# Optimization experiments

Measured on AMD Instinct MI355X. Metric: run time of the kernel, lower is better.

## Reference

```python
import jax, jax.numpy as jnp
import numpy as np


def _knn_graph(x, k):
    """Faithful port of DynamicLstmGnn.knn_to_graph + get_u_v, returning the
    dense symmetrized edge-weight matrix [N, N] (the original re-sparsifies
    this same matrix via coalesce; nonzero extraction is data-dependent and
    not jit-able, so the dense matrix is the canonical output)."""
    N = x.shape[0]
    # negative squared euclidean distance: -||xi||^2 + 2 xi.xj - ||xj||^2
    xx = jnp.sum(x * x, axis=1, keepdims=True)          # [N, 1]
    inner = -2.0 * (x @ x.T)                              # [N, N]
    pairwise_distance = -xx - inner - xx.T                # [N, N], <= 0
    vals, idx = jax.lax.top_k(pairwise_distance, k)       # [N, k] largest (= closest)
    rows = jnp.repeat(jnp.arange(N), k)                   # idx_prime.flatten()
    # sparse COO -> to_dense (duplicate indices sum, matching torch.sparse)
    edges = jnp.zeros((N, N), dtype=x.dtype).at[rows, idx.ravel()].add(vals.ravel())
    edges_int = (edges > 0).astype(x.dtype)
    reflected_int = edges_int + edges_int.T
    reflected_edges = edges + edges.T
    denom = jnp.where(reflected_int == 0, jnp.ones((), x.dtype), reflected_int)
    edges = reflected_edges / denom
    diag = jnp.arange(N)
    edges = edges.at[diag, diag].set(0.0)                 # fill_diagonal_(0)
    return edges


def setup_inputs() -> dict:
    key = jax.random.key(0)
    x = jax.random.normal(key, (10000, 64), dtype=jnp.float32)
    return {"x": x, "k": 5}


def reference(x, k):
    return _knn_graph(x, k)
```

## Files before the change

kernel.cpp:

```cpp
#include <hip/hip_runtime.h>

#define D 64
#define K 5
#define LK 8
#define GK 12
#define NSPLIT 16
#define NTILES 625
#define ROWBLK 157
#define NCOMP (ROWBLK * NSPLIT)
typedef unsigned int u32;
typedef unsigned long long u64;
typedef __bf16 bf16x8 __attribute__((ext_vector_type(8)));
typedef float  f32x4v __attribute__((ext_vector_type(4)));

__device__ __forceinline__ u32 med3u(u32 a, u32 b, u32 c) {
    u32 r;
    asm("v_med3_u32 %0, %1, %2, %3" : "=v"(r) : "v"(a), "v"(b), "v"(c));
    return r;
}

__device__ __forceinline__ u32 pack32(float v, int idx) {
    u32 u = __float_as_uint(v);
    u ^= ((u32)((int)u >> 31)) | 0x80000000u;
    return (u & 0xFFFFC000u) | ((~(u32)idx) & 0x3FFFu);
}
__device__ __forceinline__ int idx32(u32 key) { return (int)((~key) & 0x3FFFu); }

__device__ __forceinline__ u64 packKV(float v, int idx) {
    u32 u = __float_as_uint(v);
    u ^= ((u32)((int)u >> 31)) | 0x80000000u;
    return ((u64)u << 32) | (u32)(~idx);
}
__device__ __forceinline__ float unpackV(u64 key) {
    u32 hu = (u32)(key >> 32);
    return (hu & 0x80000000u) ? __uint_as_float(hu & 0x7fffffffu)
                              : __uint_as_float(~hu);
}

template<int LO, int LA, int LB, typename T>
__device__ __forceinline__ void mergeKeep(T a[LA], const T b[LB]) {
    T A[LA], B[LB], out[LO];
#pragma unroll
    for (int i = 0; i < LA; ++i) A[i] = a[i];
#pragma unroll
    for (int i = 0; i < LB; ++i) B[i] = b[i];
#pragma unroll
    for (int m = 0; m < LO; ++m) {
        bool ta = A[0] >= B[0];
        out[m] = ta ? A[0] : B[0];
#pragma unroll
        for (int i = 0; i < LA - 1; ++i) A[i] = ta ? A[i + 1] : A[i];
        A[LA - 1] = ta ? (T)0 : A[LA - 1];
#pragma unroll
        for (int i = 0; i < LB - 1; ++i) B[i] = ta ? B[i] : B[i + 1];
        B[LB - 1] = ta ? B[LB - 1] : (T)0;
    }
#pragma unroll
    for (int m = 0; m < LO; ++m) a[m] = out[m];
}

__global__ __launch_bounds__(256) void prep(
    const float* __restrict__ x, __bf16* __restrict__ xbA, float* __restrict__ xxf, int N)
{
    int g = blockIdx.x * 256 + threadIdx.x;
    const int REPACK = NTILES * 2 * 64;
    if (g < REPACK) {
        int tile = g >> 7;
        int rem  = g & 127;
        int kh   = rem >> 6;
        int lane = rem & 63;
        int q = lane >> 4, r = lane & 15;
        int row = tile * 16 + r;
        int k0  = kh * 32 + q * 8;
        const float4* p = (const float4*)(x + (size_t)row * D + k0);
        float4 v0 = p[0], v1 = p[1];
        bf16x8 o;
        o[0] = (__bf16)v0.x; o[1] = (__bf16)v0.y; o[2] = (__bf16)v0.z; o[3] = (__bf16)v0.w;
        o[4] = (__bf16)v1.x; o[5] = (__bf16)v1.y; o[6] = (__bf16)v1.z; o[7] = (__bf16)v1.w;
        ((bf16x8*)xbA)[g] = o;
        return;
    }
    int i = g - REPACK;
    if (i >= N) return;
    const float4* p = (const float4*)(x + (size_t)i * D);
    float s = 0.f;
#pragma unroll
    for (int t = 0; t < 16; ++t) {
        float4 v = p[t];
        s += v.x * v.x + v.y * v.y + v.z * v.z + v.w * v.w;
    }
    xxf[i] = s;
}

__global__ __launch_bounds__(256, 6) void topk_zero_mfma(
    const __bf16* __restrict__ xbA, const float* __restrict__ xxf, int N,
    u32* __restrict__ wsK, float* __restrict__ outZ, long long totalF4,
    int nZero, int f4PerZ)
{
    const int bx  = blockIdx.x;
    const int tid = threadIdx.x;
    const int g8  = bx >> 3;
    const int r8  = bx & 7;

    if (g8 % 6 == 0) {
        int zid = (g8 / 6) * 8 + r8;
        if (zid >= nZero) return;
        long long s = (long long)zid * f4PerZ;
        long long e = s + f4PerZ; if (e > totalF4) e = totalF4;
        const f32x4v z = {0.f, 0.f, 0.f, 0.f};
        for (long long i = s + tid; i < e; i += 256)
            __builtin_nontemporal_store(z, (f32x4v*)(outZ + 4 * i));
        return;
    }

    const int cid = bx - (g8 / 6 + 1) * 8;
    if (cid >= NCOMP) return;
    const int split = cid / ROWBLK;
    const int rb    = cid - split * ROWBLK;

    const int lane = tid & 63;
    const int wave = tid >> 6;
    const int l15  = lane & 15;
    const int q    = lane >> 4;
    const int r0 = rb * 64 + wave * 16;

    const bf16x8* fb = (const bf16x8*)xbA;

    int bt = r0 >> 4; if (bt > NTILES - 1) bt = NTILES - 1;
    const bf16x8 B0 = fb[bt * 128 + lane];
    const bf16x8 B1 = fb[bt * 128 + 64 + lane];

    const bf16x8* ap = fb + (size_t)split * 128 + lane;
    const float* xcp = xxf + split * 16 + q * 4;
    int cbase = split * 16 + q * 4;
    const int apBump = NSPLIT * 128;
    const int xcBump = NSPLIT * 16;

    u32 L[LK];
#pragma unroll
    for (int m = 0; m < LK; ++m) L[m] = 0u;

    bf16x8 A0a = ap[0];
    bf16x8 A1a = ap[64];
    f32x4v xca = *(const f32x4v*)xcp;
    ap += apBump; xcp += xcBump;
    bf16x8 A0b = ap[0];
    bf16x8 A1b = ap[64];
    f32x4v xcb = *(const f32x4v*)xcp;

    for (int t = split; t < NTILES; t += NSPLIT) {
        ap += apBump; xcp += xcBump;
        const bf16x8 nA0 = ap[0];
        const bf16x8 nA1 = ap[64];
        const f32x4v nxc = *(const f32x4v*)xcp;

        f32x4v acc0 = {0.f, 0.f, 0.f, 0.f};
        f32x4v acc1 = {0.f, 0.f, 0.f, 0.f};
        acc0 = __builtin_amdgcn_mfma_f32_16x16x32_bf16(A0a, B0, acc0, 0, 0, 0);
        acc1 = __builtin_amdgcn_mfma_f32_16x16x32_bf16(A1a, B1, acc1, 0, 0, 0);

#pragma unroll
        for (int v = 0; v < 4; ++v) {
            float dk = fmaf(-0.5f, xca[v], acc0[v] + acc1[v]);
            u32 key = pack32(dk, cbase + v);
            u32 n0 = max(L[0], key);
            u32 n1 = med3u(L[0], L[1], key);
            u32 n2 = med3u(L[1], L[2], key);
            u32 n3 = med3u(L[2], L[3], key);
            u32 n4 = med3u(L[3], L[4], key);
            u32 n5 = med3u(L[4], L[5], key);
            u32 n6 = med3u(L[5], L[6], key);
            u32 n7 = med3u(L[6], L[7], key);
            L[0]=n0; L[1]=n1; L[2]=n2; L[3]=n3; L[4]=n4; L[5]=n5; L[6]=n6; L[7]=n7;
        }
        cbase += xcBump;
        A0a = A0b; A1a = A1b; xca = xcb;
        A0b = nA0; A1b = nA1; xcb = nxc;
    }

#pragma unroll
    for (int mask = 16; mask <= 32; mask <<= 1) {
        u32 P[LK];
#pragma unroll
        for (int m = 0; m < LK; ++m) P[m] = (u32)__shfl_xor((int)L[m], mask);
        mergeKeep<LK, LK, LK, u32>(L, P);
    }

    if (lane < 16) {
        int row = r0 + l15;
        if (row < N) {
            u32* dst = wsK + ((size_t)row * NSPLIT + split) * LK;
#pragma unroll
            for (int m = 0; m < LK; ++m) dst[m] = L[m];
        }
    }
}

__global__ __launch_bounds__(256) void rescore_scatter(
    const u32* __restrict__ wsK, const float* __restrict__ x, const float* __restrict__ xxf,
    float* __restrict__ out, int N)
{
    const int lane = threadIdx.x & 63;
    const int wave = threadIdx.x >> 6;
    const int sub  = lane & 3;
    const int row  = blockIdx.x * 64 + wave * 16 + (lane >> 2);
    const bool vrow = (row < N);
    const int rr = vrow ? row : 0;

    u32 cur[GK];
    {
        const u32* Lp = wsK + ((size_t)rr * NSPLIT + 4 * sub) * LK;
#pragma unroll
        for (int m = 0; m < LK; ++m) cur[m] = Lp[m];
#pragma unroll
        for (int m = LK; m < GK; ++m) cur[m] = 0u;
#pragma unroll
        for (int l = 1; l < 4; ++l) {
            u32 b[LK];
#pragma unroll
            for (int m = 0; m < LK; ++m) b[m] = Lp[l * LK + m];
            mergeKeep<GK, GK, LK, u32>(cur, b);
        }
    }
#pragma unroll
    for (int mask = 1; mask <= 2; mask <<= 1) {
        u32 P[GK];
#pragma unroll
        for (int m = 0; m < GK; ++m) P[m] = (u32)__shfl_xor((int)cur[m], mask);
        mergeKeep<GK, GK, GK, u32>(cur, P);
    }

    const float nxi = xxf[rr];
    int   cj[3]; bool cval[3];
    float d[3] = {0.f, 0.f, 0.f};
    const f32x4v* pj[3];
#pragma unroll
    for (int c = 0; c < 3; ++c) {
        int j = idx32(cur[sub * 3 + c]);
        cval[c] = (j < N) && (cur[sub * 3 + c] != 0u);
        cj[c] = cval[c] ? j : 0;
        pj[c] = (const f32x4v*)(x + (size_t)cj[c] * D);
    }
    const f32x4v* xip = (const f32x4v*)(x + (size_t)rr * D);
#pragma unroll
    for (int t = 0; t < 16; ++t) {
        const f32x4v xv = xip[t];
#pragma unroll
        for (int c = 0; c < 3; ++c) {
            const f32x4v pv = pj[c][t];
            d[c] = fmaf(xv[0], pv[0], d[c]);
            d[c] = fmaf(xv[1], pv[1], d[c]);
            d[c] = fmaf(xv[2], pv[2], d[c]);
            d[c] = fmaf(xv[3], pv[3], d[c]);
        }
    }
    u64 F[K];
#pragma unroll
    for (int c = 0; c < 3; ++c) {
        float val = 2.f * d[c] - nxi - xxf[cj[c]];
        F[c] = cval[c] ? packKV(val, cj[c]) : 0ull;
    }
    F[3] = 0ull; F[4] = 0ull;
    { u64 a0=F[0],a1=F[1],a2=F[2];
      if (a0 < a1) { u64 t0=a0; a0=a1; a1=t0; }
      if (a1 < a2) { u64 t0=a1; a1=a2; a2=t0; }
      if (a0 < a1) { u64 t0=a0; a0=a1; a1=t0; }
      F[0]=a0; F[1]=a1; F[2]=a2; }
#pragma unroll
    for (int mask = 1; mask <= 2; mask <<= 1) {
        u64 P[K];
#pragma unroll
        for (int m = 0; m < K; ++m) P[m] = __shfl_xor(F[m], mask);
        mergeKeep<K, K, K, u64>(F, P);
    }

    if (sub == 0 && vrow) {
#pragma unroll
        for (int m = 0; m < K; ++m) {
            int j = (int)(~(u32)F[m]);
            if ((unsigned)j < (unsigned)N && j != row) {
                float v = unpackV(F[m]);
                atomicAdd(out + (size_t)row * N + j, v);
                atomicAdd(out + (size_t)j * N + row, v);
            }
        }
    }
}

extern "C" void kernel_launch(void* const* d_in, const int* in_sizes, int n_in,
                              void* d_out, int out_size, void* d_ws, size_t ws_size,
                              hipStream_t stream) {
    const float* x = (const float*)d_in[0];
    const int N = in_sizes[0] / D;
    float* out = (float*)d_out;

    const size_t oXB = 0;
    const size_t oXX = 0x150000;
    const size_t oWK = 0x160000;
    __bf16* xbA = (__bf16*)((char*)d_ws + oXB);
    float*  xxf = (float*)((char*)d_ws + oXX);
    u32*    wsK = (u32*)((char*)d_ws + oWK);

    const int prepThreads = NTILES * 2 * 64 + N;
    prep<<<(prepThreads + 255) / 256, 256, 0, stream>>>(x, xbA, xxf, N);

    long long totalF4 = (long long)out_size / 4;
    const int nBlocksTotal = 3024;
    const int nZero = 504;
    int f4PerZ = (int)((totalF4 + nZero - 1) / nZero);
    topk_zero_mfma<<<nBlocksTotal, 256, 0, stream>>>(
        xbA, xxf, N, wsK, out, totalF4, nZero, f4PerZ);

    rescore_scatter<<<ROWBLK, 256, 0, stream>>>(wsK, x, xxf, out, N);
}
```

Measured before the change: 451.2 us.

## Seed MFMA accumulator with -0.5*norm and chain both MFMAs into one accumulator

Prep now also writes a precomputed -0.5*||x||^2 array, which the top-k kernel uses as the initial MFMA accumulator. The two MFMAs chain into that single accumulator, which removes the separate add and fma per element. The packed key index is built incrementally from a decreasing base instead of through pack32. The double-buffered prefetch is cut to a single stage. The launch-bounds occupancy hint of 6 is dropped, and the zero-fill uses plain stores instead of nontemporal ones. The chained MFMAs add a dependency, which may expose MFMA latency now that the prefetch is shallower.

```diff
diff --git a/kernel.cpp b/kernel.cpp
--- a/kernel.cpp
+++ b/kernel.cpp
@@ -60,7 +60,8 @@
 }
 
 __global__ __launch_bounds__(256) void prep(
-    const float* __restrict__ x, __bf16* __restrict__ xbA, float* __restrict__ xxf, int N)
+    const float* __restrict__ x, __bf16* __restrict__ xbA,
+    float* __restrict__ xxf, float* __restrict__ xxh, int N)
 {
     int g = blockIdx.x * 256 + threadIdx.x;
     const int REPACK = NTILES * 2 * 64;
@@ -90,10 +91,11 @@
         s += v.x * v.x + v.y * v.y + v.z * v.z + v.w * v.w;
     }
     xxf[i] = s;
-}
-
-__global__ __launch_bounds__(256, 6) void topk_zero_mfma(
-    const __bf16* __restrict__ xbA, const float* __restrict__ xxf, int N,
+    xxh[i] = -0.5f * s;
+}
+
+__global__ __launch_bounds__(256) void topk_zero_mfma(
+    const __bf16* __restrict__ xbA, const float* __restrict__ xxh, int N,
     u32* __restrict__ wsK, float* __restrict__ outZ, long long totalF4,
     int nZero, int f4PerZ)
 {
@@ -109,7 +111,7 @@
         long long e = s + f4PerZ; if (e > totalF4) e = totalF4;
         const f32x4v z = {0.f, 0.f, 0.f, 0.f};
         for (long long i = s + tid; i < e; i += 256)
-            __builtin_nontemporal_store(z, (f32x4v*)(outZ + 4 * i));
+            *(f32x4v*)(outZ + 4 * i) = z;
         return;
     }
 
@@ -131,8 +133,8 @@
     const bf16x8 B1 = fb[bt * 128 + 64 + lane];
 
     const bf16x8* ap = fb + (size_t)split * 128 + lane;
-    const float* xcp = xxf + split * 16 + q * 4;
-    int cbase = split * 16 + q * 4;
+    const float* xhp = xxh + split * 16 + q * 4;
+    u32 base16k = 0x3FFFu - (u32)(split * 16 + q * 4);
     const int apBump = NSPLIT * 128;
     const int xcBump = NSPLIT * 16;
 
@@ -140,29 +142,25 @@
 #pragma unroll
     for (int m = 0; m < LK; ++m) L[m] = 0u;
 
-    bf16x8 A0a = ap[0];
-    bf16x8 A1a = ap[64];
-    f32x4v xca = *(const f32x4v*)xcp;
-    ap += apBump; xcp += xcBump;
-    bf16x8 A0b = ap[0];
-    bf16x8 A1b = ap[64];
-    f32x4v xcb = *(const f32x4v*)xcp;
+    bf16x8 A0 = ap[0];
+    bf16x8 A1 = ap[64];
+    f32x4v xh = *(const f32x4v*)xhp;
 
     for (int t = split; t < NTILES; t += NSPLIT) {
-        ap += apBump; xcp += xcBump;
+        ap += apBump; xhp += xcBump;
         const bf16x8 nA0 = ap[0];
         const bf16x8 nA1 = ap[64];
-        const f32x4v nxc = *(const f32x4v*)xcp;
-
-        f32x4v acc0 = {0.f, 0.f, 0.f, 0.f};
-        f32x4v acc1 = {0.f, 0.f, 0.f, 0.f};
-        acc0 = __builtin_amdgcn_mfma_f32_16x16x32_bf16(A0a, B0, acc0, 0, 0, 0);
-        acc1 = __builtin_amdgcn_mfma_f32_16x16x32_bf16(A1a, B1, acc1, 0, 0, 0);
+        const f32x4v nxh = *(const f32x4v*)xhp;
+
+        f32x4v acc = xh;
+        acc = __builtin_amdgcn_mfma_f32_16x16x32_bf16(A0, B0, acc, 0, 0, 0);
+        acc = __builtin_amdgcn_mfma_f32_16x16x32_bf16(A1, B1, acc, 0, 0, 0);
 
 #pragma unroll
         for (int v = 0; v < 4; ++v) {
-            float dk = fmaf(-0.5f, xca[v], acc0[v] + acc1[v]);
-            u32 key = pack32(dk, cbase + v);
+            u32 u = __float_as_uint(acc[v]);
+            u ^= ((u32)((int)u >> 31)) | 0x80000000u;
+            u32 key = (u & 0xFFFFC000u) | (base16k - (u32)v);
             u32 n0 = max(L[0], key);
             u32 n1 = med3u(L[0], L[1], key);
             u32 n2 = med3u(L[1], L[2], key);
@@ -173,9 +171,8 @@
             u32 n7 = med3u(L[6], L[7], key);
             L[0]=n0; L[1]=n1; L[2]=n2; L[3]=n3; L[4]=n4; L[5]=n5; L[6]=n6; L[7]=n7;
         }
-        cbase += xcBump;
-        A0a = A0b; A1a = A1b; xca = xcb;
-        A0b = nA0; A1b = nA1; xcb = nxc;
+        base16k -= (u32)xcBump;
+        A0 = nA0; A1 = nA1; xh = nxh;
     }
 
 #pragma unroll
@@ -296,20 +293,22 @@
 
     const size_t oXB = 0;
     const size_t oXX = 0x150000;
-    const size_t oWK = 0x160000;
+    const size_t oXH = 0x160000;
+    const size_t oWK = 0x170000;
     __bf16* xbA = (__bf16*)((char*)d_ws + oXB);
     float*  xxf = (float*)((char*)d_ws + oXX);
+    float*  xxh = (float*)((char*)d_ws + oXH);
     u32*    wsK = (u32*)((char*)d_ws + oWK);
 
     const int prepThreads = NTILES * 2 * 64 + N;
-    prep<<<(prepThreads + 255) / 256, 256, 0, stream>>>(x, xbA, xxf, N);
+    prep<<<(prepThreads + 255) / 256, 256, 0, stream>>>(x, xbA, xxf, xxh, N);
 
     long long totalF4 = (long long)out_size / 4;
     const int nBlocksTotal = 3024;
     const int nZero = 504;
     int f4PerZ = (int)((totalF4 + nZero - 1) / nZero);
     topk_zero_mfma<<<nBlocksTotal, 256, 0, stream>>>(
-        xbA, xxf, N, wsK, out, totalF4, nZero, f4PerZ);
+        xbA, xxh, N, wsK, out, totalF4, nZero, f4PerZ);
 
     rescore_scatter<<<ROWBLK, 256, 0, stream>>>(wsK, x, xxf, out, N);
 }
```

New measurement: 445.2 us. No clear change (-1.3%).
